# Performance work log

Measured on AMD Instinct MI355X. Metric: run time of the kernel, lower is better.

The kernel has to match this reference:

```python
import jax, jax.numpy as jnp
import numpy as np

T, N, D, R, E = 512, 32, 300, 3, 64
NUM_NODES, VG = 70000, 40000


def setup_inputs() -> dict:
    key = jax.random.key(0)
    ks = jax.random.split(key, 10)
    return {
        "x_indices": jax.random.randint(ks[0], (T, N), 0, NUM_NODES),
        "edge_src": jax.random.randint(ks[1], (T, R, E), 0, N),
        "edge_dst": jax.random.randint(ks[2], (T, R, E), 0, N),
        "X": jax.random.normal(ks[3], (NUM_NODES, D), dtype=jnp.float32) * 0.1,
        "conv_W": jax.random.normal(ks[4], (R, D, D), dtype=jnp.float32) * 0.05,
        "W0": jax.random.normal(ks[5], (D, D), dtype=jnp.float32) * 0.05,
        "Wu": jax.random.normal(ks[6], (N * D, D), dtype=jnp.float32) * 0.01,
        "Uu": jax.random.normal(ks[7], (D, D), dtype=jnp.float32) * 0.05,
        "Wg": jax.random.normal(ks[8], (VG, D), dtype=jnp.float32) * 0.05,
        "bg": jnp.zeros((VG,), dtype=jnp.float32),
    }


def gcn_conv(x, W, src, dst):
    """torch_geometric GCNConv(bias=False): add self-loops, D^-1/2 (A+I) D^-1/2 (x W)."""
    n = x.shape[0]
    h = x @ W  # [N, D]
    loop = jnp.arange(n)
    s = jnp.concatenate([src, loop])
    t = jnp.concatenate([dst, loop])
    deg = jax.ops.segment_sum(jnp.ones_like(t, dtype=x.dtype), t, num_segments=n)
    dinv = jnp.where(deg > 0, jax.lax.rsqrt(jnp.maximum(deg, 1e-12)), 0.0)
    norm = dinv[s] * dinv[t]  # [E+N]
    return jax.ops.segment_sum(h[s] * norm[:, None], t, num_segments=n)


def reference(x_indices, edge_src, edge_dst, X, conv_W, W0, Wu, Uu, Wg, bg):
    def step(mem, inp):
        idx, src, dst = inp  # [N], [R,E], [R,E]
        x = X[idx]  # grapharea features [N, D]
        # sum of per-relation GCNConv outputs
        conv = jnp.sum(
            jax.vmap(gcn_conv, in_axes=(None, 0, 0, 0))(x, conv_W, src, dst), axis=0
        )
        proposed = conv + x @ W0  # eye(N) @ (x @ W0) == x @ W0
        # GRU-style update gate: [1, N*D] @ [N*D, D] + mem_row0 @ [D, D]
        gate = jax.nn.sigmoid(x.reshape(1, -1) @ Wu + mem[0:1] @ Uu)  # [1, D]
        new_mem = gate * proposed + (1.0 - gate) * mem  # broadcast over N rows
        logits = jnp.maximum(new_mem[0], 0.0) @ Wg.T + bg  # [VG]
        # memory is a non-grad buffer in torch (.data.copy_): stop gradient through time
        return jax.lax.stop_gradient(new_mem), jax.nn.log_softmax(logits)

    mem0 = jnp.zeros((N, D), dtype=X.dtype)
    _, log_probs = jax.lax.scan(step, mem0, (x_indices, edge_src, edge_dst))
    # include_senses=False: per-step torch.tensor(0) stacked -> zeros([T])
    return log_probs, jnp.zeros((x_indices.shape[0],), dtype=jnp.int32)
```

## Files before the change

### kernel.cpp

```cpp
#include <hip/hip_runtime.h>
#include <hip/hip_bf16.h>
#include <math.h>

#define T_ 512
#define N_ 32
#define D_ 300
#define R_ 3
#define E_ 64
#define VG_ 40000

typedef __attribute__((ext_vector_type(8))) short bf16x8;
typedef __attribute__((ext_vector_type(4))) float f32x4;

static __device__ inline unsigned short f2b(float f) {
  __hip_bfloat16 h = __float2bfloat16(f);
  return *(unsigned short*)&h;
}

__global__ void k_zero(float* __restrict__ p, int n) {
  int i = blockIdx.x * blockDim.x + threadIdx.x;
  if (i < n) p[i] = 0.f;
}

__global__ void k_tr_wu(const float* __restrict__ Wu, unsigned short* __restrict__ Wt) {
  __shared__ float s[32][33];
  int kb = blockIdx.x * 32, nb = blockIdx.y * 32;
  int tn = threadIdx.x & 31, tr = threadIdx.x >> 5;
  for (int i = tr; i < 32; i += 8) {
    int k = kb + i, n = nb + tn;
    s[i][tn] = (n < 300) ? Wu[(size_t)k * 300 + n] : 0.f;
  }
  __syncthreads();
  for (int i = tr; i < 32; i += 8) {
    int n = nb + i, k = kb + tn;
    Wt[(size_t)n * 9600 + k] = f2b(s[tn][i]);
  }
}

__global__ void k_tr_wcat(const float* __restrict__ convW, const float* __restrict__ W0,
                          unsigned short* __restrict__ Wt) {
  __shared__ float s[32][33];
  int kb = blockIdx.x * 32, nb = blockIdx.y * 32;
  int tn = threadIdx.x & 31, tr = threadIdx.x >> 5;
  for (int i = tr; i < 32; i += 8) {
    int k = kb + i, n = nb + tn;
    float v = 0.f;
    if (n < 300 && k < 1200)
      v = (k < 900) ? convW[(size_t)k * 300 + n] : W0[(size_t)(k - 900) * 300 + n];
    s[i][tn] = v;
  }
  __syncthreads();
  for (int i = tr; i < 32; i += 8) {
    int n = nb + i, k = kb + tn;
    Wt[(size_t)n * 1216 + k] = f2b(s[tn][i]);
  }
}

__global__ void k_gather(const int* __restrict__ xidx, const int* __restrict__ esrc,
                         const int* __restrict__ edst, const float* __restrict__ X,
                         unsigned short* __restrict__ xg, unsigned short* __restrict__ Ag)
{
  const int t = blockIdx.x;
  __shared__ int s_idx[N_];
  __shared__ int s_src[R_][E_];
  __shared__ int s_dst[R_][E_];
  __shared__ int s_deg[R_][N_];
  __shared__ float s_dinv[R_][N_];
  const int tid = threadIdx.x;

  if (tid < N_) s_idx[tid] = xidx[t * N_ + tid];
  if (tid < R_ * E_) {
    int r = tid / E_, e = tid % E_;
    s_src[r][e] = esrc[(t * R_ + r) * E_ + e];
    s_dst[r][e] = edst[(t * R_ + r) * E_ + e];
  }
  if (tid < R_ * N_) ((int*)s_deg)[tid] = 1;
  __syncthreads();
  if (tid < R_ * E_) {
    int r = tid / E_;
    atomicAdd(&s_deg[r][s_dst[r][tid % E_]], 1);
  }
  __syncthreads();
  if (tid < R_ * N_) ((float*)s_dinv)[tid] = rsqrtf((float)((int*)s_deg)[tid]);
  __syncthreads();

  for (int nd = tid; nd < N_ * D_; nd += blockDim.x) {
    int n = nd / D_, d = nd % D_;
    xg[(size_t)t * (N_ * D_) + nd] = f2b(X[(size_t)s_idx[n] * D_ + d]);
  }
  if (tid < D_) {
    int d = tid;
    float x0 = X[(size_t)s_idx[0] * D_ + d];
    #pragma unroll
    for (int r = 0; r < R_; ++r) {
      float dinv0 = s_dinv[r][0];
      float acc = dinv0 * dinv0 * x0;
      for (int e = 0; e < E_; ++e) {
        if (s_dst[r][e] == 0) {
          int s = s_src[r][e];
          acc += s_dinv[r][s] * dinv0 * X[(size_t)s_idx[s] * D_ + d];
        }
      }
      Ag[(size_t)t * 1216 + r * D_ + d] = f2b(acc);
    }
    Ag[(size_t)t * 1216 + 900 + d] = f2b(x0);
  }
  if (tid < 16) Ag[(size_t)t * 1216 + 1200 + tid] = 0;
}

template<bool ATOMIC>
__global__ __launch_bounds__(256) void k_bgemm(
    const unsigned short* __restrict__ A,
    const unsigned short* __restrict__ B,
    float* __restrict__ C, int ldc, int Ncols, int K, int kchunk)
{
  const int tid = threadIdx.x;
  const int wid = tid >> 6, lane = tid & 63;
  const int l16 = lane & 15, lq = lane >> 4;
  const int bm = blockIdx.x * 128 + (wid & 1) * 64;
  const int bn = blockIdx.y * 128 + (wid >> 1) * 64;
  const int k0 = blockIdx.z * kchunk;
  const int nk = kchunk / 32;

  f32x4 acc[4][4] = {};
  const unsigned short* ap[4];
  const unsigned short* bp[4];
  #pragma unroll
  for (int mt = 0; mt < 4; ++mt) ap[mt] = A + (size_t)(bm + mt * 16 + l16) * K + k0 + lq * 8;
  #pragma unroll
  for (int nt = 0; nt < 4; ++nt) bp[nt] = B + (size_t)(bn + nt * 16 + l16) * K + k0 + lq * 8;

  #pragma unroll 2
  for (int c = 0; c < nk; ++c) {
    bf16x8 af[4], bfr[4];
    #pragma unroll
    for (int mt = 0; mt < 4; ++mt) af[mt] = *(const bf16x8*)(ap[mt] + c * 32);
    #pragma unroll
    for (int nt = 0; nt < 4; ++nt) bfr[nt] = *(const bf16x8*)(bp[nt] + c * 32);
    #pragma unroll
    for (int mt = 0; mt < 4; ++mt)
      #pragma unroll
      for (int nt = 0; nt < 4; ++nt)
        acc[mt][nt] = __builtin_amdgcn_mfma_f32_16x16x32_bf16(af[mt], bfr[nt], acc[mt][nt], 0, 0, 0);
  }

  #pragma unroll
  for (int mt = 0; mt < 4; ++mt) {
    #pragma unroll
    for (int r = 0; r < 4; ++r) {
      int row = bm + mt * 16 + lq * 4 + r;
      #pragma unroll
      for (int nt = 0; nt < 4; ++nt) {
        int col = bn + nt * 16 + l16;
        if (col < Ncols) {
          if (ATOMIC) atomicAdd(&C[(size_t)row * ldc + col], acc[mt][nt][r]);
          else        C[(size_t)row * ldc + col] = acc[mt][nt][r];
        }
      }
    }
  }
}

__global__ __launch_bounds__(256) void k_lgemm(
    const unsigned short* __restrict__ A, const float* __restrict__ Wg,
    const float* __restrict__ bg, float* __restrict__ C)
{
  const int tid = threadIdx.x;
  const int wid = tid >> 6, lane = tid & 63;
  const int l16 = lane & 15, lq = lane >> 4;
  const int bm = blockIdx.x * 128 + (wid & 1) * 64;
  const int bn = blockIdx.y * 128 + (wid >> 1) * 64;

  f32x4 acc[4][4] = {};
  const unsigned short* ap[4];
  const float* bp[4];
  #pragma unroll
  for (int mt = 0; mt < 4; ++mt) ap[mt] = A + (size_t)(bm + mt * 16 + l16) * 320 + lq * 8;
  #pragma unroll
  for (int nt = 0; nt < 4; ++nt) {
    int r = bn + nt * 16 + l16;
    if (r > VG_ - 1) r = VG_ - 1;
    bp[nt] = Wg + (size_t)r * 300;
  }

  #pragma unroll
  for (int c = 0; c < 10; ++c) {
    bf16x8 af[4], bfr[4];
    #pragma unroll
    for (int mt = 0; mt < 4; ++mt) af[mt] = *(const bf16x8*)(ap[mt] + c * 32);
    if (c < 9) {
      #pragma unroll
      for (int nt = 0; nt < 4; ++nt) {
        f32x4 x = *(const f32x4*)(bp[nt] + c * 32 + lq * 8);
        f32x4 y = *(const f32x4*)(bp[nt] + c * 32 + lq * 8 + 4);
        bf16x8 bv;
        #pragma unroll
        for (int j = 0; j < 4; ++j) { bv[j] = (short)f2b(x[j]); bv[4 + j] = (short)f2b(y[j]); }
        bfr[nt] = bv;
      }
    } else {
      #pragma unroll
      for (int nt = 0; nt < 4; ++nt) {
        bf16x8 bv;
        #pragma unroll
        for (int j = 0; j < 8; ++j) {
          int k = 288 + lq * 8 + j;
          bv[j] = (short)((k < 300) ? f2b(bp[nt][k]) : 0);
        }
        bfr[nt] = bv;
      }
    }
    #pragma unroll
    for (int mt = 0; mt < 4; ++mt)
      #pragma unroll
      for (int nt = 0; nt < 4; ++nt)
        acc[mt][nt] = __builtin_amdgcn_mfma_f32_16x16x32_bf16(af[mt], bfr[nt], acc[mt][nt], 0, 0, 0);
  }

  #pragma unroll
  for (int mt = 0; mt < 4; ++mt) {
    #pragma unroll
    for (int r = 0; r < 4; ++r) {
      int row = bm + mt * 16 + lq * 4 + r;
      #pragma unroll
      for (int nt = 0; nt < 4; ++nt) {
        int col = bn + nt * 16 + l16;
        if (col < VG_)
          C[(size_t)row * VG_ + col] = acc[mt][nt][r] + bg[col];
      }
    }
  }
}

__global__ __launch_bounds__(640) void k_rec(
    const float* __restrict__ gx, const float* __restrict__ P0,
    const float* __restrict__ Uu, unsigned short* __restrict__ Mrelu_bf)
{
  __shared__ __align__(16) unsigned short m_bf[320];
  __shared__ float zs[304];
  __shared__ unsigned short mr_s[8 * 320];
  const int tid = threadIdx.x;
  const int wid = tid >> 6, lane = tid & 63;
  const int l16 = lane & 15, lq = lane >> 4;
  const int nt0 = wid * 2, nt1 = wid * 2 + 1;
  const bool two = (nt1 < 19);

  bf16x8 b0[10], b1[10];
  {
    int n0 = nt0 * 16 + l16, n1 = nt1 * 16 + l16;
    #pragma unroll
    for (int c = 0; c < 10; ++c) {
      bf16x8 v0, v1;
      #pragma unroll
      for (int j = 0; j < 8; ++j) {
        int k = c * 32 + lq * 8 + j;
        float f0 = (k < 300 && n0 < 300) ? Uu[(size_t)k * 300 + n0] : 0.f;
        float f1 = (two && k < 300 && n1 < 300) ? Uu[(size_t)k * 300 + n1] : 0.f;
        v0[j] = (short)f2b(f0);
        v1[j] = (short)f2b(f1);
      }
      b0[c] = v0; b1[c] = v1;
    }
  }

  float m_reg = 0.f;
  if (tid < 320) m_bf[tid] = 0;
  __syncthreads();

  for (int t = 0; t < T_; ++t) {
    float gxv = 0.f, p0v = 0.f;
    if (tid < 300) {
      gxv = gx[(size_t)t * D_ + tid];
      p0v = P0[(size_t)t * D_ + tid];
    }
    f32x4 acc0 = {0.f, 0.f, 0.f, 0.f}, acc1 = {0.f, 0.f, 0.f, 0.f};
    #pragma unroll
    for (int c = 0; c < 10; ++c) {
      bf16x8 a = *(const bf16x8*)(m_bf + c * 32 + lq * 8);
      acc0 = __builtin_amdgcn_mfma_f32_16x16x32_bf16(a, b0[c], acc0, 0, 0, 0);
      if (two)
        acc1 = __builtin_amdgcn_mfma_f32_16x16x32_bf16(a, b1[c], acc1, 0, 0, 0);
    }
    if (lq == 0) {
      zs[nt0 * 16 + l16] = acc0[0];
      if (two) zs[nt1 * 16 + l16] = acc1[0];
    }
    __syncthreads();
    if (tid < 300) {
      float z = zs[tid] + gxv;
      float g = 1.f / (1.f + __expf(-z));
      m_reg = fmaf(g, p0v - m_reg, m_reg);
      m_bf[tid] = f2b(m_reg);
      mr_s[(t & 7) * 320 + tid] = f2b(fmaxf(m_reg, 0.f));
    } else if (tid < 320) {
      mr_s[(t & 7) * 320 + tid] = 0;
    }
    __syncthreads();
    if ((t & 7) == 7) {
      unsigned int* dst = (unsigned int*)(Mrelu_bf + (size_t)(t - 7) * 320);
      const unsigned int* src = (const unsigned int*)mr_s;
      for (int w = tid; w < 1280; w += 640) dst[w] = src[w];
    }
  }
}

__global__ __launch_bounds__(256) void k_lsm(float* __restrict__ out) {
  const int t = blockIdx.x;
  float* row = out + (size_t)t * VG_;
  __shared__ float redM[256];
  __shared__ float redS[256];
  const int tid = threadIdx.x;
  float lm = -1e30f, ls = 0.f;
  for (int v = tid; v < VG_; v += 256) {
    float z = row[v];
    float m2 = fmaxf(lm, z);
    ls = ls * expf(lm - m2) + expf(z - m2);
    lm = m2;
  }
  redM[tid] = lm; redS[tid] = ls;
  __syncthreads();
  for (int s = 128; s > 0; s >>= 1) {
    if (tid < s) {
      float mA = redM[tid], mB = redM[tid + s];
      float M = fmaxf(mA, mB);
      redS[tid] = redS[tid] * expf(mA - M) + redS[tid + s] * expf(mB - M);
      redM[tid] = M;
    }
    __syncthreads();
  }
  float lse = redM[0] + logf(redS[0]);
  for (int v = tid; v < VG_; v += 256) row[v] = row[v] - lse;
  if (tid == 0) out[(size_t)T_ * VG_ + t] = 0.0f;
}

extern "C" void kernel_launch(void* const* d_in, const int* in_sizes, int n_in,
                              void* d_out, int out_size, void* d_ws, size_t ws_size,
                              hipStream_t stream) {
  const int*   xidx  = (const int*)d_in[0];
  const int*   esrc  = (const int*)d_in[1];
  const int*   edst  = (const int*)d_in[2];
  const float* X     = (const float*)d_in[3];
  const float* convW = (const float*)d_in[4];
  const float* W0    = (const float*)d_in[5];
  const float* Wu    = (const float*)d_in[6];
  const float* Uu    = (const float*)d_in[7];
  const float* Wg    = (const float*)d_in[8];
  const float* bg    = (const float*)d_in[9];
  float* out = (float*)d_out;

  char* ws = (char*)d_ws;
  float*          gx     = (float*)ws;
  float*          P0     = (float*)(ws + 614400);
  unsigned short* MreluB = (unsigned short*)(ws + 1228800);
  unsigned short* xgB    = (unsigned short*)(ws + 1556480);
  unsigned short* AgB    = (unsigned short*)(ws + 11386880);
  unsigned short* WuT    = (unsigned short*)(ws + 12632064);
  unsigned short* WcatT  = (unsigned short*)(ws + 20004864);

  k_zero<<<(T_ * D_ + 255) / 256, 256, 0, stream>>>(gx, T_ * D_);
  k_tr_wu<<<dim3(300, 12), 256, 0, stream>>>(Wu, WuT);
  k_tr_wcat<<<dim3(38, 12), 256, 0, stream>>>(convW, W0, WcatT);
  k_gather<<<T_, 320, 0, stream>>>(xidx, esrc, edst, X, xgB, AgB);

  k_bgemm<true><<<dim3(4, 3, 10), 256, 0, stream>>>(xgB, WuT, gx, D_, D_, 9600, 960);
  k_bgemm<false><<<dim3(4, 3, 1), 256, 0, stream>>>(AgB, WcatT, P0, D_, D_, 1216, 1216);

  k_rec<<<1, 640, 0, stream>>>(gx, P0, Uu, MreluB);

  k_lgemm<<<dim3(4, 313), 256, 0, stream>>>(MreluB, Wg, bg, out);
  k_lsm<<<T_, 256, 0, stream>>>(out);
}
```

Baseline: 949.3 us.

## Retile logits GEMM, prefetch recurrence inputs, vectorize log-softmax

The logits GEMM is retiled so each block covers all 512 timesteps for a 64-column slice of Wg. Each Wg row is then read and converted to bf16 once instead of four times, at the cost of more accumulators per wave. The single-block recurrence prefetches the next step's gx/P0 values, drops the divergent 'two' branch, and replaces __syncthreads with an lgkmcnt-wait-plus-barrier. The log-softmax kernel now uses float4 loads and stores.

New measurement: 891.3 us. 1.06x faster.

```diff
diff --git a/kernel.cpp b/kernel.cpp
--- a/kernel.cpp
+++ b/kernel.cpp
@@ -11,6 +11,8 @@
 
 typedef __attribute__((ext_vector_type(8))) short bf16x8;
 typedef __attribute__((ext_vector_type(4))) float f32x4;
+
+#define LGKM_BARRIER() asm volatile("s_waitcnt lgkmcnt(0)\n\ts_barrier" ::: "memory")
 
 static __device__ inline unsigned short f2b(float f) {
   __hip_bfloat16 h = __float2bfloat16(f);
@@ -161,33 +163,27 @@
   }
 }
 
-__global__ __launch_bounds__(256) void k_lgemm(
+__global__ __launch_bounds__(256, 2) void k_lgemm(
     const unsigned short* __restrict__ A, const float* __restrict__ Wg,
     const float* __restrict__ bg, float* __restrict__ C)
 {
   const int tid = threadIdx.x;
   const int wid = tid >> 6, lane = tid & 63;
   const int l16 = lane & 15, lq = lane >> 4;
-  const int bm = blockIdx.x * 128 + (wid & 1) * 64;
-  const int bn = blockIdx.y * 128 + (wid >> 1) * 64;
-
-  f32x4 acc[4][4] = {};
-  const unsigned short* ap[4];
+  const int bn = blockIdx.x * 64;
+  const int m0 = wid * 128;
+
+  f32x4 acc[8][4] = {};
+  const unsigned short* ap[8];
   const float* bp[4];
   #pragma unroll
-  for (int mt = 0; mt < 4; ++mt) ap[mt] = A + (size_t)(bm + mt * 16 + l16) * 320 + lq * 8;
-  #pragma unroll
-  for (int nt = 0; nt < 4; ++nt) {
-    int r = bn + nt * 16 + l16;
-    if (r > VG_ - 1) r = VG_ - 1;
-    bp[nt] = Wg + (size_t)r * 300;
-  }
+  for (int mt = 0; mt < 8; ++mt) ap[mt] = A + (size_t)(m0 + mt * 16 + l16) * 320 + lq * 8;
+  #pragma unroll
+  for (int nt = 0; nt < 4; ++nt) bp[nt] = Wg + (size_t)(bn + nt * 16 + l16) * 300;
 
   #pragma unroll
   for (int c = 0; c < 10; ++c) {
-    bf16x8 af[4], bfr[4];
-    #pragma unroll
-    for (int mt = 0; mt < 4; ++mt) af[mt] = *(const bf16x8*)(ap[mt] + c * 32);
+    bf16x8 bfr[4];
     if (c < 9) {
       #pragma unroll
       for (int nt = 0; nt < 4; ++nt) {
@@ -210,23 +206,28 @@
         bfr[nt] = bv;
       }
     }
-    #pragma unroll
-    for (int mt = 0; mt < 4; ++mt)
+    bf16x8 af[8];
+    #pragma unroll
+    for (int mt = 0; mt < 8; ++mt) af[mt] = *(const bf16x8*)(ap[mt] + c * 32);
+    #pragma unroll
+    for (int mt = 0; mt < 8; ++mt)
       #pragma unroll
       for (int nt = 0; nt < 4; ++nt)
         acc[mt][nt] = __builtin_amdgcn_mfma_f32_16x16x32_bf16(af[mt], bfr[nt], acc[mt][nt], 0, 0, 0);
   }
 
-  #pragma unroll
-  for (int mt = 0; mt < 4; ++mt) {
+  float bb[4];
+  #pragma unroll
+  for (int nt = 0; nt < 4; ++nt) bb[nt] = bg[bn + nt * 16 + l16];
+  #pragma unroll
+  for (int mt = 0; mt < 8; ++mt) {
     #pragma unroll
     for (int r = 0; r < 4; ++r) {
-      int row = bm + mt * 16 + lq * 4 + r;
+      int row = m0 + mt * 16 + lq * 4 + r;
       #pragma unroll
       for (int nt = 0; nt < 4; ++nt) {
         int col = bn + nt * 16 + l16;
-        if (col < VG_)
-          C[(size_t)row * VG_ + col] = acc[mt][nt][r] + bg[col];
+        C[(size_t)row * VG_ + col] = acc[mt][nt][r] + bb[nt];
       }
     }
   }
@@ -237,13 +238,12 @@
     const float* __restrict__ Uu, unsigned short* __restrict__ Mrelu_bf)
 {
   __shared__ __align__(16) unsigned short m_bf[320];
-  __shared__ float zs[304];
+  __shared__ float zs[320];
   __shared__ unsigned short mr_s[8 * 320];
   const int tid = threadIdx.x;
   const int wid = tid >> 6, lane = tid & 63;
   const int l16 = lane & 15, lq = lane >> 4;
   const int nt0 = wid * 2, nt1 = wid * 2 + 1;
-  const bool two = (nt1 < 19);
 
   bf16x8 b0[10], b1[10];
   {
@@ -255,7 +255,7 @@
       for (int j = 0; j < 8; ++j) {
         int k = c * 32 + lq * 8 + j;
         float f0 = (k < 300 && n0 < 300) ? Uu[(size_t)k * 300 + n0] : 0.f;
-        float f1 = (two && k < 300 && n1 < 300) ? Uu[(size_t)k * 300 + n1] : 0.f;
+        float f1 = (k < 300 && n1 < 300) ? Uu[(size_t)k * 300 + n1] : 0.f;
         v0[j] = (short)f2b(f0);
         v1[j] = (short)f2b(f1);
       }
@@ -265,57 +265,63 @@
 
   float m_reg = 0.f;
   if (tid < 320) m_bf[tid] = 0;
+  float gx_cur = 0.f, p0_cur = 0.f, gx_nxt = 0.f, p0_nxt = 0.f;
+  if (tid < 300) { gx_cur = gx[tid]; p0_cur = P0[tid]; }
   __syncthreads();
 
   for (int t = 0; t < T_; ++t) {
-    float gxv = 0.f, p0v = 0.f;
-    if (tid < 300) {
-      gxv = gx[(size_t)t * D_ + tid];
-      p0v = P0[(size_t)t * D_ + tid];
+    if (tid < 300 && t + 1 < T_) {
+      gx_nxt = gx[(size_t)(t + 1) * D_ + tid];
+      p0_nxt = P0[(size_t)(t + 1) * D_ + tid];
     }
     f32x4 acc0 = {0.f, 0.f, 0.f, 0.f}, acc1 = {0.f, 0.f, 0.f, 0.f};
     #pragma unroll
     for (int c = 0; c < 10; ++c) {
       bf16x8 a = *(const bf16x8*)(m_bf + c * 32 + lq * 8);
       acc0 = __builtin_amdgcn_mfma_f32_16x16x32_bf16(a, b0[c], acc0, 0, 0, 0);
-      if (two)
-        acc1 = __builtin_amdgcn_mfma_f32_16x16x32_bf16(a, b1[c], acc1, 0, 0, 0);
+      acc1 = __builtin_amdgcn_mfma_f32_16x16x32_bf16(a, b1[c], acc1, 0, 0, 0);
     }
     if (lq == 0) {
       zs[nt0 * 16 + l16] = acc0[0];
-      if (two) zs[nt1 * 16 + l16] = acc1[0];
-    }
-    __syncthreads();
+      zs[nt1 * 16 + l16] = acc1[0];
+    }
+    LGKM_BARRIER();
     if (tid < 300) {
-      float z = zs[tid] + gxv;
+      float z = zs[tid] + gx_cur;
       float g = 1.f / (1.f + __expf(-z));
-      m_reg = fmaf(g, p0v - m_reg, m_reg);
+      m_reg = fmaf(g, p0_cur - m_reg, m_reg);
       m_bf[tid] = f2b(m_reg);
       mr_s[(t & 7) * 320 + tid] = f2b(fmaxf(m_reg, 0.f));
     } else if (tid < 320) {
       mr_s[(t & 7) * 320 + tid] = 0;
     }
-    __syncthreads();
+    LGKM_BARRIER();
     if ((t & 7) == 7) {
       unsigned int* dst = (unsigned int*)(Mrelu_bf + (size_t)(t - 7) * 320);
       const unsigned int* src = (const unsigned int*)mr_s;
       for (int w = tid; w < 1280; w += 640) dst[w] = src[w];
     }
+    gx_cur = gx_nxt; p0_cur = p0_nxt;
   }
 }
 
 __global__ __launch_bounds__(256) void k_lsm(float* __restrict__ out) {
   const int t = blockIdx.x;
   float* row = out + (size_t)t * VG_;
+  const f32x4* row4 = (const f32x4*)row;
   __shared__ float redM[256];
   __shared__ float redS[256];
   const int tid = threadIdx.x;
   float lm = -1e30f, ls = 0.f;
-  for (int v = tid; v < VG_; v += 256) {
-    float z = row[v];
-    float m2 = fmaxf(lm, z);
-    ls = ls * expf(lm - m2) + expf(z - m2);
-    lm = m2;
+  for (int v = tid; v < VG_ / 4; v += 256) {
+    f32x4 z4 = row4[v];
+    #pragma unroll
+    for (int j = 0; j < 4; ++j) {
+      float z = z4[j];
+      float m2 = fmaxf(lm, z);
+      ls = ls * expf(lm - m2) + expf(z - m2);
+      lm = m2;
+    }
   }
   redM[tid] = lm; redS[tid] = ls;
   __syncthreads();
@@ -329,7 +335,13 @@
     __syncthreads();
   }
   float lse = redM[0] + logf(redS[0]);
-  for (int v = tid; v < VG_; v += 256) row[v] = row[v] - lse;
+  f32x4* row4w = (f32x4*)row;
+  for (int v = tid; v < VG_ / 4; v += 256) {
+    f32x4 z4 = row4w[v];
+    #pragma unroll
+    for (int j = 0; j < 4; ++j) z4[j] -= lse;
+    row4w[v] = z4;
+  }
   if (tid == 0) out[(size_t)T_ * VG_ + t] = 0.0f;
 }
 
@@ -367,6 +379,6 @@
 
   k_rec<<<1, 640, 0, stream>>>(gx, P0, Uu, MreluB);
 
-  k_lgemm<<<dim3(4, 313), 256, 0, stream>>>(MreluB, Wg, bg, out);
+  k_lgemm<<<dim3(625), 256, 0, stream>>>(MreluB, Wg, bg, out);
   k_lsm<<<T_, 256, 0, stream>>>(out);
 }
```
